# Kernel tuning notes

Measured on AMD Instinct MI355X. Metric: run time of the kernel, lower is better.

The kernel has to match this reference:

```python
import jax, jax.numpy as jnp
import numpy as np

B, T, E, H = 8, 2048, 1024, 64  # batch, seq_len(=block_size), embedding_size, head_size


def setup_inputs() -> dict:
    key = jax.random.key(0)
    k1, k2, k3, k4, k5 = jax.random.split(key, 5)
    x = jax.random.normal(k1, (B, T, E), dtype=jnp.float32)
    Wk = jax.random.normal(k2, (H, E), dtype=jnp.float32) * 0.02
    Wq = jax.random.normal(k3, (H, E), dtype=jnp.float32) * 0.02
    Wv = jax.random.normal(k4, (H, E), dtype=jnp.float32) * 0.02
    attention_mask = jax.random.randint(k5, (B, T), 0, 2).astype(jnp.int32)
    return {"x": x, "Wk": Wk, "Wq": Wq, "Wv": Wv, "attention_mask": attention_mask}


def reference(x, Wk, Wq, Wv, attention_mask):
    # Linear projections (nn.Linear with no bias: y = x @ W.T)
    k = jnp.einsum('bte,he->bth', x, Wk)
    q = jnp.einsum('bte,he->bth', x, Wq)
    v = jnp.einsum('bte,he->bth', x, Wv)
    scale = v.shape[2] ** -0.5  # head_size^-0.5, faithful to v.shape[2]**(-0.5)
    wei = jnp.einsum('bqh,bkh->bqk', q, k) * scale  # [B,T,T]
    # Causal mask (tril buffer) AND padding outer-product mask; the double-precision
    # outer product in the original just tests nonzero-ness, so a boolean AND is exact.
    causal = jnp.tril(jnp.ones((T, T), dtype=bool))  # [T,T]
    pad = (attention_mask[:, :, None] * attention_mask[:, None, :]) != 0  # [B,T,T]
    wei = jnp.where(causal[None, :, :] & pad, wei, -jnp.inf)
    wei = jax.nn.softmax(wei, axis=-1)
    wei = jnp.nan_to_num(wei)  # fully-masked rows -> 0 (matches torch.nan_to_num)
    # dropout in eval mode -> identity
    out = jnp.einsum('bqk,bkh->bqh', wei, v)
    return out
```

## Files before the change

kernel.cpp:

```cpp
#include <hip/hip_runtime.h>
#include <hip/hip_bf16.h>

typedef __bf16 bf16x8 __attribute__((ext_vector_type(8)));
typedef __bf16 bf16x4 __attribute__((ext_vector_type(4)));
typedef float  f32x4  __attribute__((ext_vector_type(4)));

#define LDP 72

__global__ __launch_bounds__(256) void wconv_kernel(
    const float* __restrict__ Wk, const float* __restrict__ Wq,
    const float* __restrict__ Wv, __bf16* __restrict__ wbf)
{
    int idx = blockIdx.x * 256 + threadIdx.x;
    int row = idx >> 8;
    int c4  = idx & 255;
    const float* wp = (row < 64) ? Wk + (size_t)row * 1024
                    : (row < 128) ? Wq + (size_t)(row - 64) * 1024
                                  : Wv + (size_t)(row - 128) * 1024;
    float4 f = *reinterpret_cast<const float4*>(wp + c4 * 4);
    bf16x4 v; v[0] = (__bf16)f.x; v[1] = (__bf16)f.y; v[2] = (__bf16)f.z; v[3] = (__bf16)f.w;
    *reinterpret_cast<bf16x4*>(&wbf[(size_t)row * 1024 + c4 * 4]) = v;
}

__global__ __launch_bounds__(1024) void proj_kernel(
    const float* __restrict__ x, const __bf16* __restrict__ wbf,
    __bf16* __restrict__ kbuf, __bf16* __restrict__ qbuf, __bf16* __restrict__ vtbuf)
{
    __shared__ __align__(16) __bf16 Slds[2][256 * LDP];
    __shared__ __align__(16) __bf16 Vtl[64 * LDP];

    const int tid  = threadIdx.x;
    const int lane = tid & 63;
    const int wid  = tid >> 6;
    const int wm   = wid >> 2;
    const int wn   = wid & 3;
    const int mbase = blockIdx.x * 64;

    const int cl = lane & 15;
    const int e0 = (lane >> 4) * 8;
    const int r0 = (lane >> 4) * 4;

    const int arow = tid >> 4, acg = tid & 15;
    const float* aptr = x + (size_t)(mbase + arow) * 1024 + acg * 4;

    float4 a0, a1;
    bf16x4 w0[3], w1[3];

#define ISSUE(aset, wset, kb) { \
    aset = *reinterpret_cast<const float4*>(aptr + (kb)); \
    _Pragma("unroll") \
    for (int i_ = 0; i_ < 3; i_++) { \
        int c_ = i_ * 1024 + tid; \
        wset[i_] = *reinterpret_cast<const bf16x4*>(&wbf[(size_t)(c_ >> 4) * 1024 + (kb) + (c_ & 15) * 4]); \
    } }

#define COMMIT(aset, wset, bufi) { \
    bf16x4 av_; \
    av_[0] = (__bf16)aset.x; av_[1] = (__bf16)aset.y; av_[2] = (__bf16)aset.z; av_[3] = (__bf16)aset.w; \
    *reinterpret_cast<bf16x4*>(&Slds[bufi][arow * LDP + acg * 4]) = av_; \
    _Pragma("unroll") \
    for (int i_ = 0; i_ < 3; i_++) { \
        int c_ = i_ * 1024 + tid; \
        *reinterpret_cast<bf16x4*>(&Slds[bufi][(64 + (c_ >> 4)) * LDP + (c_ & 15) * 4]) = wset[i_]; \
    } }

    f32x4 acc[3];
    #pragma unroll
    for (int n = 0; n < 3; n++) acc[n] = (f32x4){0.f, 0.f, 0.f, 0.f};

    ISSUE(a0, w0, 0);
    ISSUE(a1, w1, 64);
    COMMIT(a0, w0, 0);
    __syncthreads();

    #pragma unroll
    for (int j = 0; j < 16; j++) {
        const __bf16* buf = Slds[j & 1];
        #pragma unroll
        for (int kk = 0; kk < 2; kk++) {
            bf16x8 a = *reinterpret_cast<const bf16x8*>(&buf[(wm * 16 + cl) * LDP + kk * 32 + e0]);
            #pragma unroll
            for (int nf = 0; nf < 3; nf++) {
                bf16x8 b = *reinterpret_cast<const bf16x8*>(&buf[(64 + wn * 48 + nf * 16 + cl) * LDP + kk * 32 + e0]);
                acc[nf] = __builtin_amdgcn_mfma_f32_16x16x32_bf16(a, b, acc[nf], 0, 0, 0);
            }
        }
        if (j < 15) {
            if (j < 14) {
                if (j & 1) { ISSUE(a1, w1, (j + 2) * 64); }
                else       { ISSUE(a0, w0, (j + 2) * 64); }
            }
            if (j & 1) { COMMIT(a0, w0, 0); }
            else       { COMMIT(a1, w1, 1); }
        }
        __syncthreads();
    }
#undef ISSUE
#undef COMMIT

    #pragma unroll
    for (int nf = 0; nf < 3; nf++) {
        int c = wn * 48 + nf * 16 + cl;
        #pragma unroll
        for (int r = 0; r < 4; r++) {
            int mrel = wm * 16 + r0 + r;
            float v = acc[nf][r];
            if (c < 64)        kbuf[(size_t)(mbase + mrel) * 64 + c]         = (__bf16)v;
            else if (c < 128)  qbuf[(size_t)(mbase + mrel) * 64 + (c - 64)]  = (__bf16)v;
            else               Vtl[(c - 128) * LDP + mrel]                   = (__bf16)v;
        }
    }
    __syncthreads();
    {
        int b   = mbase >> 11;
        int tof = mbase & 2047;
        int h   = tid >> 4;
        int seg = tid & 15;
        bf16x4 v4 = *reinterpret_cast<const bf16x4*>(&Vtl[h * LDP + seg * 4]);
        *reinterpret_cast<bf16x4*>(&vtbuf[(size_t)b * 64 * 2048 + (size_t)h * 2048 + tof + seg * 4]) = v4;
    }
}

__global__ __launch_bounds__(256) void attn_kernel(
    const __bf16* __restrict__ qbuf, const __bf16* __restrict__ kbuf,
    const __bf16* __restrict__ vtbuf, const int* __restrict__ mask,
    float* __restrict__ out, float* __restrict__ accpart, float* __restrict__ mlpart,
    int nsplit, int tps)
{
    __shared__ __align__(16) __bf16 Klds[64 * LDP];
    __shared__ __align__(16) __bf16 Vlds[64 * LDP];
    __shared__ __align__(16) __bf16 Plds[4][16 * LDP];

    const int tid  = threadIdx.x;
    const int lane = tid & 63;
    const int w    = tid >> 6;
    const int qt   = blockIdx.x;
    const int sp   = blockIdx.y;
    const int b    = blockIdx.z;
    const int qbase = qt * 64 + w * 16;

    const int jbeg = sp * tps;
    const int jend = min((sp + 1) * tps, qt + 1);

    if (nsplit > 1 && jbeg >= jend) {
        float* ap = accpart + ((size_t)(b * nsplit + sp) * 2048 + qt * 64) * 64;
        for (int i = tid; i < 64 * 64; i += 256) ap[i] = 0.f;
        float* mp = mlpart + ((size_t)(b * nsplit + sp) * 2048 + qt * 64) * 2;
        for (int i = tid; i < 64; i += 256) { mp[2 * i] = -INFINITY; mp[2 * i + 1] = 0.f; }
        return;
    }

    const int cl = lane & 15;
    const int e0 = (lane >> 4) * 8;
    const int r0 = (lane >> 4) * 4;

    bf16x8 aq[2];
    #pragma unroll
    for (int kk = 0; kk < 2; kk++)
        aq[kk] = *reinterpret_cast<const bf16x8*>(&qbuf[((size_t)b * 2048 + qbase + cl) * 64 + kk * 32 + e0]);

    float ms[4], ls[4];
    f32x4 acc[4];
    #pragma unroll
    for (int r = 0; r < 4; r++) { ms[r] = -INFINITY; ls[r] = 0.f; }
    #pragma unroll
    for (int hf = 0; hf < 4; hf++) acc[hf] = (f32x4){0.f, 0.f, 0.f, 0.f};

    const int srow = tid >> 3;
    const int scg  = tid & 7;

    for (int j = jbeg; j < jend; j++) {
        #pragma unroll
        for (int p = 0; p < 2; p++) {
            int rr = p * 32 + srow;
            *reinterpret_cast<bf16x8*>(&Klds[rr * LDP + scg * 8]) =
                *reinterpret_cast<const bf16x8*>(&kbuf[((size_t)b * 2048 + j * 64 + rr) * 64 + scg * 8]);
            *reinterpret_cast<bf16x8*>(&Vlds[rr * LDP + scg * 8]) =
                *reinterpret_cast<const bf16x8*>(&vtbuf[(size_t)b * 64 * 2048 + (size_t)rr * 2048 + j * 64 + scg * 8]);
        }
        __syncthreads();

        f32x4 s[4];
        #pragma unroll
        for (int jf = 0; jf < 4; jf++) {
            f32x4 t = (f32x4){0.f, 0.f, 0.f, 0.f};
            #pragma unroll
            for (int kk = 0; kk < 2; kk++) {
                bf16x8 bk = *reinterpret_cast<const bf16x8*>(&Klds[(jf * 16 + cl) * LDP + kk * 32 + e0]);
                t = __builtin_amdgcn_mfma_f32_16x16x32_bf16(aq[kk], bk, t, 0, 0, 0);
            }
            s[jf] = t;
        }

        float tmax[4] = {-INFINITY, -INFINITY, -INFINITY, -INFINITY};
        #pragma unroll
        for (int jf = 0; jf < 4; jf++) {
            int kv = j * 64 + jf * 16 + cl;
            int mk = mask[b * 2048 + kv];
            #pragma unroll
            for (int r = 0; r < 4; r++) {
                float sv = s[jf][r] * 0.125f;
                bool ok = (mk != 0) && (kv <= qbase + r0 + r);
                sv = ok ? sv : -INFINITY;
                s[jf][r] = sv;
                tmax[r] = fmaxf(tmax[r], sv);
            }
        }

        #pragma unroll
        for (int r = 0; r < 4; r++) {
            #pragma unroll
            for (int off = 1; off < 16; off <<= 1)
                tmax[r] = fmaxf(tmax[r], __shfl_xor(tmax[r], off));
            float mn = fmaxf(ms[r], tmax[r]);
            float alpha = (mn == -INFINITY) ? 1.0f : __expf(ms[r] - mn);
            float rs = 0.f;
            #pragma unroll
            for (int jf = 0; jf < 4; jf++) {
                float p = (mn == -INFINITY) ? 0.f : __expf(s[jf][r] - mn);
                s[jf][r] = p;
                rs += p;
            }
            #pragma unroll
            for (int off = 1; off < 16; off <<= 1)
                rs += __shfl_xor(rs, off);
            ls[r] = ls[r] * alpha + rs;
            ms[r] = mn;
            #pragma unroll
            for (int hf = 0; hf < 4; hf++) acc[hf][r] *= alpha;
        }

        #pragma unroll
        for (int jf = 0; jf < 4; jf++)
            #pragma unroll
            for (int r = 0; r < 4; r++)
                Plds[w][(r0 + r) * LDP + jf * 16 + cl] = (__bf16)s[jf][r];
        #pragma unroll
        for (int kk = 0; kk < 2; kk++) {
            bf16x8 ap = *reinterpret_cast<const bf16x8*>(&Plds[w][cl * LDP + kk * 32 + e0]);
            #pragma unroll
            for (int hf = 0; hf < 4; hf++) {
                bf16x8 bv = *reinterpret_cast<const bf16x8*>(&Vlds[(hf * 16 + cl) * LDP + kk * 32 + e0]);
                acc[hf] = __builtin_amdgcn_mfma_f32_16x16x32_bf16(ap, bv, acc[hf], 0, 0, 0);
            }
        }
        __syncthreads();
    }

    if (nsplit == 1) {
        #pragma unroll
        for (int hf = 0; hf < 4; hf++)
            #pragma unroll
            for (int r = 0; r < 4; r++) {
                int qrow = qbase + r0 + r;
                int mq = mask[b * 2048 + qrow];
                float l = ls[r];
                float v = (l > 0.f && mq != 0) ? acc[hf][r] / l : 0.f;
                out[((size_t)b * 2048 + qrow) * 64 + hf * 16 + cl] = v;
            }
    } else {
        #pragma unroll
        for (int hf = 0; hf < 4; hf++)
            #pragma unroll
            for (int r = 0; r < 4; r++) {
                int qrow = qbase + r0 + r;
                accpart[((size_t)(b * nsplit + sp) * 2048 + qrow) * 64 + hf * 16 + cl] = acc[hf][r];
            }
        if (cl == 0) {
            #pragma unroll
            for (int r = 0; r < 4; r++) {
                int qrow = qbase + r0 + r;
                mlpart[((size_t)(b * nsplit + sp) * 2048 + qrow) * 2 + 0] = ms[r];
                mlpart[((size_t)(b * nsplit + sp) * 2048 + qrow) * 2 + 1] = ls[r];
            }
        }
    }
}

template<int NS>
__global__ __launch_bounds__(256) void combine_kernel(
    const float* __restrict__ accpart, const float* __restrict__ mlpart,
    const int* __restrict__ mask, float* __restrict__ out)
{
    int idx = blockIdx.x * 256 + threadIdx.x;
    int qglob = idx >> 6;
    int h = idx & 63;
    int b = qglob >> 11;
    int qrow = qglob & 2047;

    if (mask[qglob] == 0) { out[idx] = 0.f; return; }

    float m_s[NS], l_s[NS];
    float M = -INFINITY;
    #pragma unroll
    for (int s = 0; s < NS; s++) {
        size_t mo = ((size_t)(b * NS + s) * 2048 + qrow) * 2;
        m_s[s] = mlpart[mo];
        l_s[s] = mlpart[mo + 1];
        M = fmaxf(M, m_s[s]);
    }
    if (M == -INFINITY) { out[idx] = 0.f; return; }

    float L = 0.f, O = 0.f;
    #pragma unroll
    for (int s = 0; s < NS; s++) {
        float wgt = (m_s[s] == -INFINITY) ? 0.f : __expf(m_s[s] - M);
        L += l_s[s] * wgt;
        O += wgt * accpart[((size_t)(b * NS + s) * 2048 + qrow) * 64 + h];
    }
    out[idx] = (L > 0.f) ? O / L : 0.f;
}

extern "C" void kernel_launch(void* const* d_in, const int* in_sizes, int n_in,
                              void* d_out, int out_size, void* d_ws, size_t ws_size,
                              hipStream_t stream) {
    const float* x  = (const float*)d_in[0];
    const float* Wk = (const float*)d_in[1];
    const float* Wq = (const float*)d_in[2];
    const float* Wv = (const float*)d_in[3];
    const int* mask = (const int*)d_in[4];
    float* out = (float*)d_out;

    const size_t NTOK = 8 * 2048;
    __bf16* kbuf  = (__bf16*)d_ws;
    __bf16* qbuf  = kbuf + NTOK * 64;
    __bf16* vtbuf = qbuf + NTOK * 64;
    __bf16* wbf   = vtbuf + (size_t)8 * 64 * 2048;
    const size_t base_bytes = NTOK * 64 * 2 * 2 + (size_t)8 * 64 * 2048 * 2
                            + (size_t)192 * 1024 * 2;

    const size_t acc_per_split = NTOK * 64 * 4;
    const size_t ml_per_split  = NTOK * 2 * 4;
    int nsplit = 1;
    if (ws_size >= base_bytes + 4 * (acc_per_split + ml_per_split))      nsplit = 4;
    else if (ws_size >= base_bytes + 2 * (acc_per_split + ml_per_split)) nsplit = 2;

    float* accpart = (float*)((char*)d_ws + base_bytes);
    float* mlpart  = accpart + NTOK * 64 * nsplit;

    wconv_kernel<<<192, 256, 0, stream>>>(Wk, Wq, Wv, wbf);
    proj_kernel<<<256, 1024, 0, stream>>>(x, wbf, kbuf, qbuf, vtbuf);
    attn_kernel<<<dim3(32, nsplit, 8), 256, 0, stream>>>(
        qbuf, kbuf, vtbuf, mask, out, accpart, mlpart, nsplit, 32 / nsplit);
    if (nsplit == 4)
        combine_kernel<4><<<(16384 * 64) / 256, 256, 0, stream>>>(accpart, mlpart, mask, out);
    else if (nsplit == 2)
        combine_kernel<2><<<(16384 * 64) / 256, 256, 0, stream>>>(accpart, mlpart, mask, out);
}
```

Before: 67.02 us.

## Double-buffer K/V tiles in attention and reorder projection prefetch with lighter barriers

The attention kernel now keeps two LDS buffers for K and V and prefetches the next-next tile into registers while computing on the current one. This replaces the load-then-sync-every-iteration pattern, with one barrier per tile after the commit. The projection kernel moves global prefetch issue to the top of each iteration, replaces __syncthreads with an lgkmcnt wait plus s_barrier, and unrolls by 2 instead of fully. The cost is roughly double the K/V LDS footprint and extra registers, which may reduce occupancy. The raw barrier relies on an lgkmcnt-only wait, and its correctness depends on global loads being consumed through registers before the LDS writes.

```diff
diff --git a/kernel.cpp b/kernel.cpp
--- a/kernel.cpp
+++ b/kernel.cpp
@@ -6,6 +6,8 @@
 typedef float  f32x4  __attribute__((ext_vector_type(4)));
 
 #define LDP 72
+
+#define BAR() { asm volatile("s_waitcnt lgkmcnt(0)" ::: "memory"); __builtin_amdgcn_s_barrier(); }
 
 __global__ __launch_bounds__(256) void wconv_kernel(
     const float* __restrict__ Wk, const float* __restrict__ Wq,
@@ -69,12 +71,16 @@
     for (int n = 0; n < 3; n++) acc[n] = (f32x4){0.f, 0.f, 0.f, 0.f};
 
     ISSUE(a0, w0, 0);
+    COMMIT(a0, w0, 0);
     ISSUE(a1, w1, 64);
-    COMMIT(a0, w0, 0);
-    __syncthreads();
-
-    #pragma unroll
+    BAR();
+
+    #pragma unroll 2
     for (int j = 0; j < 16; j++) {
+        if (j < 14) {
+            if (j & 1) { ISSUE(a1, w1, (j + 2) * 64); }
+            else       { ISSUE(a0, w0, (j + 2) * 64); }
+        }
         const __bf16* buf = Slds[j & 1];
         #pragma unroll
         for (int kk = 0; kk < 2; kk++) {
@@ -86,14 +92,10 @@
             }
         }
         if (j < 15) {
-            if (j < 14) {
-                if (j & 1) { ISSUE(a1, w1, (j + 2) * 64); }
-                else       { ISSUE(a0, w0, (j + 2) * 64); }
-            }
             if (j & 1) { COMMIT(a0, w0, 0); }
             else       { COMMIT(a1, w1, 1); }
-        }
-        __syncthreads();
+            BAR();
+        }
     }
 #undef ISSUE
 #undef COMMIT
@@ -127,8 +129,8 @@
     float* __restrict__ out, float* __restrict__ accpart, float* __restrict__ mlpart,
     int nsplit, int tps)
 {
-    __shared__ __align__(16) __bf16 Klds[64 * LDP];
-    __shared__ __align__(16) __bf16 Vlds[64 * LDP];
+    __shared__ __align__(16) __bf16 Klds[2][64 * LDP];
+    __shared__ __align__(16) __bf16 Vlds[2][64 * LDP];
     __shared__ __align__(16) __bf16 Plds[4][16 * LDP];
 
     const int tid  = threadIdx.x;
@@ -169,27 +171,49 @@
     const int srow = tid >> 3;
     const int scg  = tid & 7;
 
-    for (int j = jbeg; j < jend; j++) {
-        #pragma unroll
-        for (int p = 0; p < 2; p++) {
-            int rr = p * 32 + srow;
-            *reinterpret_cast<bf16x8*>(&Klds[rr * LDP + scg * 8]) =
-                *reinterpret_cast<const bf16x8*>(&kbuf[((size_t)b * 2048 + j * 64 + rr) * 64 + scg * 8]);
-            *reinterpret_cast<bf16x8*>(&Vlds[rr * LDP + scg * 8]) =
-                *reinterpret_cast<const bf16x8*>(&vtbuf[(size_t)b * 64 * 2048 + (size_t)rr * 2048 + j * 64 + scg * 8]);
-        }
-        __syncthreads();
+    bf16x8 sk0, sk1, sv0, sv1;
+    bf16x8 tk0, tk1, tv0, tv1;
+
+#define KV_ISSUE(S0,S1,S2,S3,jj) { \
+    size_t kb_ = ((size_t)b * 2048 + (jj) * 64 + srow) * 64 + scg * 8; \
+    S0 = *reinterpret_cast<const bf16x8*>(&kbuf[kb_]); \
+    S1 = *reinterpret_cast<const bf16x8*>(&kbuf[kb_ + (size_t)32 * 64]); \
+    size_t vb_ = (size_t)b * 64 * 2048 + (size_t)srow * 2048 + (jj) * 64 + scg * 8; \
+    S2 = *reinterpret_cast<const bf16x8*>(&vtbuf[vb_]); \
+    S3 = *reinterpret_cast<const bf16x8*>(&vtbuf[vb_ + (size_t)32 * 2048]); }
+
+#define KV_COMMIT(S0,S1,S2,S3,bi) { \
+    *reinterpret_cast<bf16x8*>(&Klds[bi][srow * LDP + scg * 8]) = S0; \
+    *reinterpret_cast<bf16x8*>(&Klds[bi][(32 + srow) * LDP + scg * 8]) = S1; \
+    *reinterpret_cast<bf16x8*>(&Vlds[bi][srow * LDP + scg * 8]) = S2; \
+    *reinterpret_cast<bf16x8*>(&Vlds[bi][(32 + srow) * LDP + scg * 8]) = S3; }
+
+    const int nt = jend - jbeg;
+    KV_ISSUE(sk0, sk1, sv0, sv1, jbeg);
+    KV_COMMIT(sk0, sk1, sv0, sv1, 0);
+    if (nt > 1) KV_ISSUE(tk0, tk1, tv0, tv1, jbeg + 1);
+    BAR();
+
+    for (int t = 0; t < nt; t++) {
+        const int cur = t & 1;
+        const int j = jbeg + t;
+        if (t + 2 < nt) {
+            if (cur) { KV_ISSUE(tk0, tk1, tv0, tv1, j + 2); }
+            else     { KV_ISSUE(sk0, sk1, sv0, sv1, j + 2); }
+        }
+        const __bf16* KL = Klds[cur];
+        const __bf16* VL = Vlds[cur];
 
         f32x4 s[4];
         #pragma unroll
         for (int jf = 0; jf < 4; jf++) {
-            f32x4 t = (f32x4){0.f, 0.f, 0.f, 0.f};
+            f32x4 tacc = (f32x4){0.f, 0.f, 0.f, 0.f};
             #pragma unroll
             for (int kk = 0; kk < 2; kk++) {
-                bf16x8 bk = *reinterpret_cast<const bf16x8*>(&Klds[(jf * 16 + cl) * LDP + kk * 32 + e0]);
-                t = __builtin_amdgcn_mfma_f32_16x16x32_bf16(aq[kk], bk, t, 0, 0, 0);
-            }
-            s[jf] = t;
+                bf16x8 bk = *reinterpret_cast<const bf16x8*>(&KL[(jf * 16 + cl) * LDP + kk * 32 + e0]);
+                tacc = __builtin_amdgcn_mfma_f32_16x16x32_bf16(aq[kk], bk, tacc, 0, 0, 0);
+            }
+            s[jf] = tacc;
         }
 
         float tmax[4] = {-INFINITY, -INFINITY, -INFINITY, -INFINITY};
@@ -240,12 +264,19 @@
             bf16x8 ap = *reinterpret_cast<const bf16x8*>(&Plds[w][cl * LDP + kk * 32 + e0]);
             #pragma unroll
             for (int hf = 0; hf < 4; hf++) {
-                bf16x8 bv = *reinterpret_cast<const bf16x8*>(&Vlds[(hf * 16 + cl) * LDP + kk * 32 + e0]);
+                bf16x8 bv = *reinterpret_cast<const bf16x8*>(&VL[(hf * 16 + cl) * LDP + kk * 32 + e0]);
                 acc[hf] = __builtin_amdgcn_mfma_f32_16x16x32_bf16(ap, bv, acc[hf], 0, 0, 0);
             }
         }
-        __syncthreads();
-    }
+
+        if (t + 1 < nt) {
+            if (cur) { KV_COMMIT(sk0, sk1, sv0, sv1, cur ^ 1); }
+            else     { KV_COMMIT(tk0, tk1, tv0, tv1, cur ^ 1); }
+            BAR();
+        }
+    }
+#undef KV_ISSUE
+#undef KV_COMMIT
 
     if (nsplit == 1) {
         #pragma unroll
```

Result: slower. 73.25 us (+9.3%).
